# Kernel tuning notes

Hardware: AMD Instinct MI355X
Metric: run time of the kernel (lower is better)

## Reference

```python
import jax, jax.numpy as jnp
import numpy as np
from jax import lax

DN = ('NCHW', 'OIHW', 'NCHW')
BN_EPS = 1e-5
LRELU_SLOPE = 0.01


def conv_block(x, w1, b1, w2, b2, gamma, bn_bias):
    # Conv2d(512->256, k=1) -> Conv2d(256->512, k=3, pad=1) -> LeakyReLU -> BatchNorm2d(512)
    y = lax.conv_general_dilated(x, w1, (1, 1), 'VALID', dimension_numbers=DN)
    y = y + b1[None, :, None, None]
    y = lax.conv_general_dilated(y, w2, (1, 1), 'SAME', dimension_numbers=DN)
    y = y + b2[None, :, None, None]
    y = jnp.where(y > 0, y, LRELU_SLOPE * y)
    # BatchNorm2d in training mode: batch statistics over (B, H, W) per channel
    mean = jnp.mean(y, axis=(0, 2, 3))
    var = jnp.var(y, axis=(0, 2, 3))
    y = (y - mean[None, :, None, None]) * lax.rsqrt(var + BN_EPS)[None, :, None, None]
    return y * gamma[None, :, None, None] + bn_bias[None, :, None, None]


def setup_inputs() -> dict:
    key = jax.random.key(0)
    ks = jax.random.split(key, 9)
    B, C, H, W = 8, 512, 32, 32
    x = jax.random.normal(ks[0], (B, C, H, W), dtype=jnp.float32)
    x1 = jax.random.normal(ks[1], (B, C, H, W), dtype=jnp.float32)
    x2 = jax.random.normal(ks[2], (B, C, H, W), dtype=jnp.float32)
    w1 = jax.random.normal(ks[3], (256, 512, 1, 1), dtype=jnp.float32) * 0.02
    b1 = jnp.zeros((256,), dtype=jnp.float32)
    w2 = jax.random.normal(ks[4], (512, 256, 3, 3), dtype=jnp.float32) * 0.02
    b2 = jnp.zeros((512,), dtype=jnp.float32)
    gamma = jnp.ones((512,), dtype=jnp.float32)
    bn_bias = jnp.zeros((512,), dtype=jnp.float32)
    beta = jax.random.normal(ks[5], (1,), dtype=jnp.float32)  # Parameter(zeros(1)) in torch; random so output is non-trivial
    return {"x": x, "x1": x1, "x2": x2, "w1": w1, "b1": b1, "w2": w2,
            "b2": b2, "gamma": gamma, "bn_bias": bn_bias, "beta": beta}


def reference(x, x1, x2, w1, b1, w2, b2, gamma, bn_bias, beta):
    B, C, H, W = x1.shape
    N = H * W
    F1 = conv_block(x1, w1, b1, w2, b2, gamma, bn_bias).reshape(B, C, N)   # [B, C, N]
    F2 = conv_block(x2, w1, b1, w2, b2, gamma, bn_bias).reshape(B, C, N)   # [B, C, N]
    scores = jnp.einsum('bcn,bdn->bcd', F1, F2)                            # [B, C, C]
    attention = jax.nn.softmax(scores, axis=-1)
    out = jnp.einsum('bcd,bdn->bcn', attention, x.reshape(B, C, N))
    return beta * out.reshape(B, C, H, W)
```

## Files before the change

### kernel.cpp

```cpp
#include <hip/hip_runtime.h>


typedef __attribute__((ext_vector_type(8))) short bfrag;
typedef __attribute__((ext_vector_type(4))) float facc;

__device__ __forceinline__ unsigned short bf16_rn(float v) {
  unsigned u = __float_as_uint(v);
  return (unsigned short)((u + 0x7fffu + ((u >> 16) & 1u)) >> 16);
}

__device__ __forceinline__ void dma16(const void* g, const void* lds) {
  __builtin_amdgcn_global_load_lds(
      (const __attribute__((address_space(1))) unsigned int*)g,
      (__attribute__((address_space(3))) unsigned int*)(unsigned int)(unsigned long long)(const char*)lds,
      16, 0, 0);
}

__global__ __launch_bounds__(256) void prologue(
    const float* __restrict__ x1, const float* __restrict__ x2,
    const float* __restrict__ w2, unsigned char* __restrict__ x12timg,
    unsigned short* __restrict__ w2s, float* __restrict__ statsz) {
  int bid = blockIdx.x;
  int t = threadIdx.x;
  if (bid < 8192) {
    __shared__ float tile[32][33];
    int p0 = (bid & 31) * 32, ci0 = ((bid >> 5) & 15) * 32, z = bid >> 9;
    const float* src = (z < 8) ? x1 + (size_t)z * 524288 : x2 + (size_t)(z - 8) * 524288;
    {
      int ci_l = t >> 5, p_l = t & 31;
#pragma unroll
      for (int j = 0; j < 4; j++)
        tile[ci_l + 8 * j][p_l] = src[(size_t)(ci0 + ci_l + 8 * j) * 1024 + p0 + p_l];
    }
    __syncthreads();
    {
      int p_l = t >> 3, cg = (t & 7) * 4;
      unsigned short hh[4], ll[4];
#pragma unroll
      for (int j = 0; j < 4; j++) {
        float v = tile[cg + j][p_l];
        hh[j] = bf16_rn(v);
        ll[j] = bf16_rn(v - __uint_as_float((unsigned)hh[j] << 16));
      }
      int px = p0 + p_l, row = px & 127, panel = px >> 7;
      int c = ci0 + cg, kc = c >> 6, ck = (c >> 3) & 7;
      int slot = ck ^ (row & 7);
      size_t byte = (((size_t)(z * 8 + panel) * 8 + kc) * 128 + row) * 256 + slot * 16 + (c & 7) * 2;
      *(ushort4*)(x12timg + byte) = make_ushort4(hh[0], hh[1], hh[2], hh[3]);
      *(ushort4*)(x12timg + byte + 128) = make_ushort4(ll[0], ll[1], ll[2], ll[3]);
    }
  } else {
    int co = bid - 8192;
    if (co < 40) statsz[co * 256 + t] = 0.f;
    int panel = co >> 7, co_l = co & 127;
    int ch = t >> 5, ci_l = t & 31;
    int chi = ci_l >> 3, cil7 = ci_l & 7;
    const float* src = w2 + ((size_t)co * 256 + t) * 9;
#pragma unroll
    for (int tap = 0; tap < 9; tap++) {
      float v = src[tap];
      unsigned short h = bf16_rn(v);
      unsigned short l = bf16_rn(v - __uint_as_float((unsigned)h << 16));
      int dy = tap / 3, slot = tap % 3;
      int e = slot * 128 + co_l;
      size_t base = (size_t)(((panel * 8 + ch) * 3 + dy)) * 24576;
      size_t off_hi = base + e * 64 + ((chi ^ (e & 7)) << 3) + cil7;
      w2s[off_hi] = h;
      w2s[off_hi ^ 32] = l;
    }
  }
}

__global__ __launch_bounds__(256) void transpose_split_x(
    const float* __restrict__ x, unsigned char* __restrict__ img) {
  __shared__ float tile[32][33];
  int z = blockIdx.z;
  const float* src = x + (size_t)z * 524288;
  int ci0 = blockIdx.y * 32, p0 = blockIdx.x * 32;
  int t = threadIdx.x;
  {
    int ci_l = t >> 5, p_l = t & 31;
#pragma unroll
    for (int j = 0; j < 4; j++)
      tile[ci_l + 8 * j][p_l] = src[(size_t)(ci0 + ci_l + 8 * j) * 1024 + p0 + p_l];
  }
  __syncthreads();
  {
    int p_l = t >> 3, cg = (t & 7) * 4;
    unsigned short hh[4], ll[4];
#pragma unroll
    for (int j = 0; j < 4; j++) {
      float v = tile[cg + j][p_l];
      hh[j] = bf16_rn(v);
      ll[j] = bf16_rn(v - __uint_as_float((unsigned)hh[j] << 16));
    }
    int px = p0 + p_l, row = px & 127, panel = px >> 7;
    int c = ci0 + cg, kc = c >> 6, ck = (c >> 3) & 7;
    int slot = ck ^ (row & 7);
    size_t byte = (((size_t)(z * 8 + panel) * 8 + kc) * 128 + row) * 256 + slot * 16 + (c & 7) * 2;
    *(ushort4*)(img + byte) = make_ushort4(hh[0], hh[1], hh[2], hh[3]);
    *(ushort4*)(img + byte + 128) = make_ushort4(ll[0], ll[1], ll[2], ll[3]);
  }
}

template <int KTOT, int EPI, int AF32, int KSPLIT>
__global__ __launch_bounds__(256, 2) void gemm_nt(
    const void* __restrict__ Asrc, long long aZS, int aKC,
    const unsigned char* __restrict__ Bimg, long long bZS, int bKC,
    void* __restrict__ out0,
    const float* __restrict__ p0, const float* __restrict__ p1,
    const float* __restrict__ p2, const float* __restrict__ p3) {
  __shared__ __attribute__((aligned(16))) unsigned char smem[49152];
  int t = threadIdx.x;
  int z = blockIdx.z;
  int zb = z, kh = 0;
  if (KSPLIT) { zb = z & 7; kh = z >> 3; }
  int m0 = blockIdx.y * 128, n0 = blockIdx.x * 64;
  int w = t >> 6, lane = t & 63;
  int lm = lane & 15, q = lane >> 4;
  int mh = (w & 1) * 64, nh = (w >> 1) * 32;
  const unsigned char* Abase = (const unsigned char*)Asrc + (size_t)zb * aZS +
      (size_t)(m0 >> 7) * ((size_t)aKC << 15) + (size_t)w * 8192 + (size_t)lane * 16;
  const unsigned char* Bbase = Bimg + (size_t)zb * bZS +
      (size_t)(n0 >> 7) * ((size_t)bKC << 15) + (size_t)(n0 & 127) * 256 +
      (size_t)w * 4096 + (size_t)lane * 16;
  facc acc[4][2] = {};
  for (int k0 = 0; k0 < KTOT; k0 += 64) {
    int kc = (KSPLIT ? kh * (KTOT / 64) : 0) + (k0 >> 6);
    __syncthreads();
    if (AF32) {
      const float* Af = (const float*)Asrc;
#pragma unroll
      for (int j = 0; j < 8; j++) {
        int idx = t + 256 * j;
        int row = idx >> 4, c4 = idx & 15;
        float4 v = *(const float4*)(Af + (size_t)(m0 + row) * KTOT + k0 + c4 * 4);
        unsigned short h0 = bf16_rn(v.x), h1 = bf16_rn(v.y), h2 = bf16_rn(v.z), h3 = bf16_rn(v.w);
        unsigned short l0 = bf16_rn(v.x - __uint_as_float((unsigned)h0 << 16));
        unsigned short l1 = bf16_rn(v.y - __uint_as_float((unsigned)h1 << 16));
        unsigned short l2 = bf16_rn(v.z - __uint_as_float((unsigned)h2 << 16));
        unsigned short l3 = bf16_rn(v.w - __uint_as_float((unsigned)h3 << 16));
        int base = row * 256 + (((c4 >> 1) ^ (row & 7)) * 16) + (c4 & 1) * 8;
        *(ushort4*)(smem + base) = make_ushort4(h0, h1, h2, h3);
        *(ushort4*)(smem + base + 128) = make_ushort4(l0, l1, l2, l3);
      }
    } else {
      const unsigned char* ap = Abase + ((size_t)kc << 15);
#pragma unroll
      for (int j = 0; j < 8; j++) dma16(ap + j * 1024, smem + w * 8192 + j * 1024);
    }
    {
      const unsigned char* bp = Bbase + ((size_t)kc << 15);
#pragma unroll
      for (int j = 0; j < 4; j++) dma16(bp + j * 1024, smem + 32768 + w * 4096 + j * 1024);
    }
    __syncthreads();
#pragma unroll
    for (int ks = 0; ks < 2; ks++) {
      bfrag ah[4], al[4], bh[2], bl[2];
#pragma unroll
      for (int mt = 0; mt < 4; mt++) {
        int m = mh + mt * 16 + lm;
        int phys = ((ks * 4 + q) ^ (m & 7)) * 16;
        const unsigned char* p = smem + m * 256 + phys;
        ah[mt] = *(const bfrag*)p;
        al[mt] = *(const bfrag*)(p + 128);
      }
#pragma unroll
      for (int nt = 0; nt < 2; nt++) {
        int n = nh + nt * 16 + lm;
        int phys = ((ks * 4 + q) ^ (n & 7)) * 16;
        const unsigned char* p = smem + 32768 + n * 256 + phys;
        bh[nt] = *(const bfrag*)p;
        bl[nt] = *(const bfrag*)(p + 128);
      }
#pragma unroll
      for (int mt = 0; mt < 4; mt++)
#pragma unroll
        for (int nt = 0; nt < 2; nt++) {
          acc[mt][nt] = __builtin_amdgcn_mfma_f32_16x16x32_bf16(ah[mt], bh[nt], acc[mt][nt], 0, 0, 0);
          acc[mt][nt] = __builtin_amdgcn_mfma_f32_16x16x32_bf16(ah[mt], bl[nt], acc[mt][nt], 0, 0, 0);
          acc[mt][nt] = __builtin_amdgcn_mfma_f32_16x16x32_bf16(al[mt], bh[nt], acc[mt][nt], 0, 0, 0);
        }
    }
  }
  if (EPI == 0) {
    unsigned char* Yimg = (unsigned char*)out0;
    int g = zb;
#pragma unroll
    for (int mt = 0; mt < 4; mt++) {
      int mb = m0 + mh + mt * 16 + q * 4;
      int ch = mb >> 5, chunk = (mb >> 3) & 3, e2 = (mb & 7) * 2;
#pragma unroll
      for (int nt = 0; nt < 2; nt++) {
        int px = n0 + nh + nt * 16 + lm;
        int gy = px >> 5, gx = px & 31;
        int slot = chunk ^ ((gx + 1) & 7);
        size_t base = ((size_t)((g * 8 + ch) * 32 + gy)) * 4096 + gx * 128 + slot * 16 + e2;
        unsigned short hh[4], ll[4];
#pragma unroll
        for (int r = 0; r < 4; r++) {
          float v = acc[mt][nt][r] + p0[mb + r];
          hh[r] = bf16_rn(v);
          ll[r] = bf16_rn(v - __uint_as_float((unsigned)hh[r] << 16));
        }
        *(ushort4*)(Yimg + base) = make_ushort4(hh[0], hh[1], hh[2], hh[3]);
        *(ushort4*)(Yimg + (base ^ 64)) = make_ushort4(ll[0], ll[1], ll[2], ll[3]);
      }
    }
  } else if (EPI == 1) {
    float* S = (float*)out0 + (size_t)kh * 2097152;
    const float* stats = p0;
    const float* rowsum = p1;
    const float* gamma = p2;
    const float* bnb = p3;
    float a2v[2], t2v[2], r2v[2];
#pragma unroll
    for (int nt = 0; nt < 2; nt++) {
      int d = n0 + nh + nt * 16 + lm;
      float mu = stats[512 + d] * (1.f / 8192.f);
      float var = stats[1536 + d] * (1.f / 8192.f) - mu * mu;
      float a = gamma[d] * rsqrtf(var + 1e-5f);
      a2v[nt] = a;
      t2v[nt] = bnb[d] - mu * a;
      r2v[nt] = rowsum[(8 + zb) * 512 + d];
    }
#pragma unroll
    for (int mt = 0; mt < 4; mt++)
#pragma unroll
      for (int r = 0; r < 4; r++) {
        int cc = m0 + mh + mt * 16 + q * 4 + r;
        float mu = stats[cc] * (1.f / 8192.f);
        float var = stats[1024 + cc] * (1.f / 8192.f) - mu * mu;
        float a1 = gamma[cc] * rsqrtf(var + 1e-5f);
        float t1 = bnb[cc] - mu * a1;
        float r1 = rowsum[zb * 512 + cc];
#pragma unroll
        for (int nt = 0; nt < 2; nt++) {
          int d = n0 + nh + nt * 16 + lm;
          float sc = a1 * a2v[nt] * acc[mt][nt][r];
          if (kh == 0)
            sc += a1 * t2v[nt] * r1 + t1 * a2v[nt] * r2v[nt] + 1024.f * t1 * t2v[nt];
          S[((size_t)(zb * 512 + cc)) * 512 + d] = sc;
        }
      }
  } else {
    float* O = (float*)out0;
    float sc = p0[0];
#pragma unroll
    for (int mt = 0; mt < 4; mt++)
#pragma unroll
      for (int r = 0; r < 4; r++) {
        int cc = m0 + mh + mt * 16 + q * 4 + r;
#pragma unroll
        for (int nt = 0; nt < 2; nt++) {
          int n = n0 + nh + nt * 16 + lm;
          O[((size_t)(zb * 512 + cc)) * 1024 + n] = sc * acc[mt][nt][r];
        }
      }
  }
}

__global__ __launch_bounds__(256, 2) void conv3x3_mfma(
    const unsigned char* __restrict__ Yimg, const unsigned short* __restrict__ w2s,
    const float* __restrict__ b2, unsigned char* __restrict__ Fimg,
    float* __restrict__ stats, float* __restrict__ rowsum) {
  __shared__ __attribute__((aligned(16))) unsigned char smem[75264];
  const int WOFF = 26112;
  int t = threadIdx.x;
  int g = blockIdx.z;
  int panel = blockIdx.y;
  int co_base = panel * 128;
  int y0 = blockIdx.x * 4;
  int w = t >> 6, lane = t & 63;
  int lm = lane & 15, q = lane >> 4;
  int co_half = (w & 1) * 64, px_half = (w >> 1) * 64;
  int px_l[4], row_l[4], x_l[4];
#pragma unroll
  for (int i = 0; i < 4; i++) {
    px_l[i] = px_half + i * 16 + lm;
    row_l[i] = px_l[i] >> 5;
    x_l[i] = px_l[i] & 31;
  }
  for (int u = t; u < 1632; u += 256)
    *(uint4*)(smem + u * 16) = make_uint4(0u, 0u, 0u, 0u);
  const unsigned char* wgbase =
      (const unsigned char*)w2s + (size_t)panel * 8 * 3 * 49152 + w * 12288 + lane * 16;
  const unsigned char* ldsw = smem + WOFF + w * 12288;
  facc acc[4][4] = {};
  for (int chunk = 0; chunk < 8; chunk++) {
    for (int dy = 0; dy < 3; dy++) {
      __syncthreads();
      {
        const unsigned char* gsrc = wgbase + (size_t)(chunk * 3 + dy) * 49152;
#pragma unroll
        for (int j = 0; j < 12; j++) dma16(gsrc + j * 1024, ldsw + j * 1024);
      }
      if (dy == 0) {
#pragma unroll
        for (int j = 0; j < 6; j++) {
          int id = w * 6 + j;
          int strip = id >> 2, part = id & 3;
          int gy = y0 - 1 + strip;
          if ((unsigned)gy < 32u) {
            const unsigned char* src = Yimg +
                ((size_t)((g * 8 + chunk) * 32 + gy)) * 4096 + part * 1024 + lane * 16;
            dma16(src, smem + strip * 4352 + 128 + part * 1024);
          }
        }
      }
      __syncthreads();
#pragma unroll
      for (int dx = 0; dx < 3; dx++) {
        bfrag ah[4], al[4], bh[4], bl[4];
#pragma unroll
        for (int j = 0; j < 4; j++) {
          int cr = co_half + j * 16 + lm;
          const unsigned char* p = smem + WOFF + dx * 16384 + cr * 128;
          int ph = (q ^ (lm & 7)) * 16;
          ah[j] = *(const bfrag*)(p + ph);
          al[j] = *(const bfrag*)(p + (ph ^ 64));
        }
#pragma unroll
        for (int i = 0; i < 4; i++) {
          int xh = x_l[i] + dx;
          int entry = (row_l[i] + dy) * 34 + xh;
          const unsigned char* p = smem + entry * 128;
          int ph = (q ^ (xh & 7)) * 16;
          bh[i] = *(const bfrag*)(p + ph);
          bl[i] = *(const bfrag*)(p + (ph ^ 64));
        }
#pragma unroll
        for (int j = 0; j < 4; j++)
#pragma unroll
          for (int i = 0; i < 4; i++) {
            acc[j][i] = __builtin_amdgcn_mfma_f32_16x16x32_bf16(ah[j], bh[i], acc[j][i], 0, 0, 0);
            acc[j][i] = __builtin_amdgcn_mfma_f32_16x16x32_bf16(ah[j], bl[i], acc[j][i], 0, 0, 0);
            acc[j][i] = __builtin_amdgcn_mfma_f32_16x16x32_bf16(al[j], bh[i], acc[j][i], 0, 0, 0);
          }
      }
    }
  }
  int grp = g >> 3;
  int px0 = blockIdx.x * 128;
#pragma unroll
  for (int j = 0; j < 4; j++) {
#pragma unroll
    for (int r = 0; r < 4; r++) {
      int co = co_base + co_half + j * 16 + q * 4 + r;
      int row = co & 127;
      float bb = b2[co];
      float s = 0.f, s2 = 0.f;
#pragma unroll
      for (int i = 0; i < 4; i++) {
        float v = acc[j][i][r] + bb;
        v = v > 0.f ? v : 0.01f * v;
        unsigned short h = bf16_rn(v);
        unsigned short l = bf16_rn(v - __uint_as_float((unsigned)h << 16));
        int px = px0 + px_l[i];
        int kc = px >> 6, ck = (px >> 3) & 7;
        int slot = ck ^ (row & 7);
        size_t byte = (((size_t)(g * 4 + panel) * 16 + kc) * 128 + row) * 256 +
                      slot * 16 + (px & 7) * 2;
        *(unsigned short*)(Fimg + byte) = h;
        *(unsigned short*)(Fimg + byte + 128) = l;
        s += v;
        s2 = fmaf(v, v, s2);
      }
#pragma unroll
      for (int d = 1; d <= 8; d <<= 1) {
        s += __shfl_xor(s, d);
        s2 += __shfl_xor(s2, d);
      }
      if (lm == 0) {
        atomicAdd(&stats[grp * 512 + co], s);
        atomicAdd(&stats[1024 + grp * 512 + co], s2);
        atomicAdd(&rowsum[g * 512 + co], s);
      }
    }
  }
}

__global__ __launch_bounds__(256) void softmax_rows(const float* __restrict__ S,
                                                    unsigned char* __restrict__ attimg) {
  int rowg = blockIdx.x;
  int z = rowg >> 9, c = rowg & 511;
  const float* p = S + (size_t)rowg * 512;
  const float* p1 = p + 2097152;
  int t = threadIdx.x;
  float2 va = *(const float2*)(p + 2 * t);
  float2 vb = *(const float2*)(p1 + 2 * t);
  float vx = va.x + vb.x, vy = va.y + vb.y;
  float mx = fmaxf(vx, vy);
#pragma unroll
  for (int d = 32; d >= 1; d >>= 1) mx = fmaxf(mx, __shfl_xor(mx, d));
  __shared__ float sred[8];
  int wave = t >> 6, lane = t & 63;
  if (lane == 0) sred[wave] = mx;
  __syncthreads();
  float m4 = fmaxf(fmaxf(sred[0], sred[1]), fmaxf(sred[2], sred[3]));
  float ex = expf(vx - m4), ey = expf(vy - m4);
  float s = ex + ey;
#pragma unroll
  for (int d = 32; d >= 1; d >>= 1) s += __shfl_xor(s, d);
  if (lane == 0) sred[4 + wave] = s;
  __syncthreads();
  float inv = 1.f / (sred[4] + sred[5] + sred[6] + sred[7]);
  float px_ = ex * inv, py_ = ey * inv;
  unsigned short h0 = bf16_rn(px_), h1 = bf16_rn(py_);
  unsigned short l0 = bf16_rn(px_ - __uint_as_float((unsigned)h0 << 16));
  unsigned short l1 = bf16_rn(py_ - __uint_as_float((unsigned)h1 << 16));
  int rowl = c & 127, panel = c >> 7;
  int d0 = 2 * t;
  int kc = d0 >> 6, ck = (d0 >> 3) & 7;
  int slot = ck ^ (rowl & 7);
  size_t byte = (((size_t)(z * 4 + panel) * 8 + kc) * 128 + rowl) * 256 +
                slot * 16 + (d0 & 7) * 2;
  *(ushort2*)(attimg + byte) = make_ushort2(h0, h1);
  *(ushort2*)(attimg + byte + 128) = make_ushort2(l0, l1);
}

extern "C" void kernel_launch(void* const* d_in, const int* in_sizes, int n_in,
                              void* d_out, int out_size, void* d_ws, size_t ws_size,
                              hipStream_t stream) {
  const float* x = (const float*)d_in[0];
  const float* x1 = (const float*)d_in[1];
  const float* x2 = (const float*)d_in[2];
  const float* w1 = (const float*)d_in[3];
  const float* b1 = (const float*)d_in[4];
  const float* w2 = (const float*)d_in[5];
  const float* b2 = (const float*)d_in[6];
  const float* gamma = (const float*)d_in[7];
  const float* bnb = (const float*)d_in[8];
  const float* beta = (const float*)d_in[9];
  float* out = (float*)d_out;
  unsigned char* wsb = (unsigned char*)d_ws;

  unsigned char* x12timg = wsb;
  unsigned char* Fimg = wsb;
  unsigned char* xtimg = wsb;
  unsigned char* attimg = wsb + 16777216;
  unsigned char* Yimg = wsb + 33554432;
  float* S = (float*)(wsb + 33554432);
  unsigned short* w2s = (unsigned short*)(wsb + 50331648);
  float* stats = (float*)(wsb + 55050240);
  float* rowsum = (float*)(wsb + 55058432);

  prologue<<<8704, 256, 0, stream>>>(x1, x2, w2, x12timg, w2s, stats);
  gemm_nt<512, 0, 1, 0><<<dim3(16, 2, 16), 256, 0, stream>>>(
      w1, 0LL, 0, x12timg, 2097152LL, 8, Yimg, b1, nullptr, nullptr, nullptr);
  conv3x3_mfma<<<dim3(8, 4, 16), 256, 0, stream>>>(
      Yimg, w2s, b2, Fimg, stats, rowsum);
  gemm_nt<512, 1, 0, 1><<<dim3(8, 4, 16), 256, 0, stream>>>(
      Fimg, 2097152LL, 16, Fimg + (size_t)8 * 2097152, 2097152LL, 16,
      S, stats, rowsum, gamma, bnb);
  transpose_split_x<<<dim3(32, 16, 8), 256, 0, stream>>>(x, xtimg);
  softmax_rows<<<4096, 256, 0, stream>>>(S, attimg);
  gemm_nt<512, 2, 0, 0><<<dim3(16, 4, 8), 256, 0, stream>>>(
      attimg, 1048576LL, 8, xtimg, 2097152LL, 8, out, beta, nullptr, nullptr, nullptr);
}
```

Measured before the change: 287.7 us.

## Load conv3x3 weights directly from global into registers and double-buffer input tiles

The prologue now writes w2 in a fragment-native layout, so each wave can load its MFMA A-operands straight from global memory into registers instead of staging them through LDS. LDS now holds only the input halo tiles, double-buffered, with the next chunk's DMA issued mid-loop, and only one barrier per chunk instead of two per dy step. This cuts LDS traffic and barrier stalls, but makes weight loads depend on global/L2 latency and bandwidth, and the 8 register fragments add VGPR pressure.

```diff
diff --git a/kernel.cpp b/kernel.cpp
--- a/kernel.cpp
+++ b/kernel.cpp
@@ -52,21 +52,19 @@
   } else {
     int co = bid - 8192;
     if (co < 40) statsz[co * 256 + t] = 0.f;
-    int panel = co >> 7, co_l = co & 127;
-    int ch = t >> 5, ci_l = t & 31;
-    int chi = ci_l >> 3, cil7 = ci_l & 7;
+    int panel = co >> 7, coh = (co >> 6) & 1, jf = (co >> 4) & 3, lmv = co & 15;
+    int chunk = t >> 5, qv = (t >> 3) & 3, e = t & 7;
+    int lanev = qv * 16 + lmv;
     const float* src = w2 + ((size_t)co * 256 + t) * 9;
 #pragma unroll
     for (int tap = 0; tap < 9; tap++) {
       float v = src[tap];
       unsigned short h = bf16_rn(v);
       unsigned short l = bf16_rn(v - __uint_as_float((unsigned)h << 16));
-      int dy = tap / 3, slot = tap % 3;
-      int e = slot * 128 + co_l;
-      size_t base = (size_t)(((panel * 8 + ch) * 3 + dy)) * 24576;
-      size_t off_hi = base + e * 64 + ((chi ^ (e & 7)) << 3) + cil7;
-      w2s[off_hi] = h;
-      w2s[off_hi ^ 32] = l;
+      int P = (panel * 8 + chunk) * 9 + tap;
+      size_t us = (((size_t)(P * 2 + coh) * 8 + jf * 2) * 512) + lanev * 8 + e;
+      w2s[us] = h;
+      w2s[us + 512] = l;
     }
   }
 }
@@ -265,8 +263,7 @@
     const unsigned char* __restrict__ Yimg, const unsigned short* __restrict__ w2s,
     const float* __restrict__ b2, unsigned char* __restrict__ Fimg,
     float* __restrict__ stats, float* __restrict__ rowsum) {
-  __shared__ __attribute__((aligned(16))) unsigned char smem[75264];
-  const int WOFF = 26112;
+  __shared__ __attribute__((aligned(16))) unsigned char smem[2][26112];
   int t = threadIdx.x;
   int g = blockIdx.z;
   int panel = blockIdx.y;
@@ -282,64 +279,59 @@
     row_l[i] = px_l[i] >> 5;
     x_l[i] = px_l[i] & 31;
   }
-  for (int u = t; u < 1632; u += 256)
-    *(uint4*)(smem + u * 16) = make_uint4(0u, 0u, 0u, 0u);
-  const unsigned char* wgbase =
-      (const unsigned char*)w2s + (size_t)panel * 8 * 3 * 49152 + w * 12288 + lane * 16;
-  const unsigned char* ldsw = smem + WOFF + w * 12288;
+  auto stageIn = [&](int ct, unsigned char* dst) {
+#pragma unroll
+    for (int jj = 0; jj < 6; jj++) {
+      int id = w * 6 + jj;
+      int strip = id >> 2, part = id & 3;
+      int gy = y0 - 1 + strip;
+      if ((unsigned)gy < 32u) {
+        const unsigned char* srcp = Yimg +
+            ((size_t)((g * 8 + ct) * 32 + gy)) * 4096 + part * 1024 + lane * 16;
+        dma16(srcp, dst + strip * 4352 + 128 + part * 1024);
+      }
+    }
+  };
+  for (int u = t; u < 3264; u += 256)
+    *(uint4*)(&smem[0][0] + (size_t)u * 16) = make_uint4(0u, 0u, 0u, 0u);
+  __syncthreads();
+  stageIn(0, &smem[0][0]);
+  __syncthreads();
+  const unsigned char* wg0 = (const unsigned char*)w2s +
+      (size_t)panel * 72 * 16384 + (size_t)(w & 1) * 8192 + (size_t)lane * 16;
   facc acc[4][4] = {};
-  for (int chunk = 0; chunk < 8; chunk++) {
-    for (int dy = 0; dy < 3; dy++) {
-      __syncthreads();
-      {
-        const unsigned char* gsrc = wgbase + (size_t)(chunk * 3 + dy) * 49152;
-#pragma unroll
-        for (int j = 0; j < 12; j++) dma16(gsrc + j * 1024, ldsw + j * 1024);
-      }
-      if (dy == 0) {
-#pragma unroll
-        for (int j = 0; j < 6; j++) {
-          int id = w * 6 + j;
-          int strip = id >> 2, part = id & 3;
-          int gy = y0 - 1 + strip;
-          if ((unsigned)gy < 32u) {
-            const unsigned char* src = Yimg +
-                ((size_t)((g * 8 + chunk) * 32 + gy)) * 4096 + part * 1024 + lane * 16;
-            dma16(src, smem + strip * 4352 + 128 + part * 1024);
-          }
+#pragma unroll 1
+  for (int c = 0; c < 8; c++) {
+    const unsigned char* bufp = &smem[c & 1][0];
+    const unsigned char* wpc = wg0 + (((size_t)c * 9) << 14);
+#pragma unroll
+    for (int r = 0; r < 9; r++) {
+      const int dy = r / 3, dx = r % 3;
+      bfrag W[8];
+#pragma unroll
+      for (int u = 0; u < 8; u++)
+        W[u] = *(const bfrag*)(wpc + (((size_t)r) << 14) + u * 1024);
+      if (r == 3 && c < 7) stageIn(c + 1, &smem[(c + 1) & 1][0]);
+      bfrag bh[4], bl[4];
+#pragma unroll
+      for (int i = 0; i < 4; i++) {
+        int xh = x_l[i] + dx;
+        int entry = (row_l[i] + dy) * 34 + xh;
+        const unsigned char* pb = bufp + entry * 128;
+        int ph = (q ^ (xh & 7)) * 16;
+        bh[i] = *(const bfrag*)(pb + ph);
+        bl[i] = *(const bfrag*)(pb + (ph ^ 64));
+      }
+#pragma unroll
+      for (int j = 0; j < 4; j++)
+#pragma unroll
+        for (int i = 0; i < 4; i++) {
+          acc[j][i] = __builtin_amdgcn_mfma_f32_16x16x32_bf16(W[2 * j], bh[i], acc[j][i], 0, 0, 0);
+          acc[j][i] = __builtin_amdgcn_mfma_f32_16x16x32_bf16(W[2 * j], bl[i], acc[j][i], 0, 0, 0);
+          acc[j][i] = __builtin_amdgcn_mfma_f32_16x16x32_bf16(W[2 * j + 1], bh[i], acc[j][i], 0, 0, 0);
         }
-      }
-      __syncthreads();
-#pragma unroll
-      for (int dx = 0; dx < 3; dx++) {
-        bfrag ah[4], al[4], bh[4], bl[4];
-#pragma unroll
-        for (int j = 0; j < 4; j++) {
-          int cr = co_half + j * 16 + lm;
-          const unsigned char* p = smem + WOFF + dx * 16384 + cr * 128;
-          int ph = (q ^ (lm & 7)) * 16;
-          ah[j] = *(const bfrag*)(p + ph);
-          al[j] = *(const bfrag*)(p + (ph ^ 64));
-        }
-#pragma unroll
-        for (int i = 0; i < 4; i++) {
-          int xh = x_l[i] + dx;
-          int entry = (row_l[i] + dy) * 34 + xh;
-          const unsigned char* p = smem + entry * 128;
-          int ph = (q ^ (xh & 7)) * 16;
-          bh[i] = *(const bfrag*)(p + ph);
-          bl[i] = *(const bfrag*)(p + (ph ^ 64));
-        }
-#pragma unroll
-        for (int j = 0; j < 4; j++)
-#pragma unroll
-          for (int i = 0; i < 4; i++) {
-            acc[j][i] = __builtin_amdgcn_mfma_f32_16x16x32_bf16(ah[j], bh[i], acc[j][i], 0, 0, 0);
-            acc[j][i] = __builtin_amdgcn_mfma_f32_16x16x32_bf16(ah[j], bl[i], acc[j][i], 0, 0, 0);
-            acc[j][i] = __builtin_amdgcn_mfma_f32_16x16x32_bf16(al[j], bh[i], acc[j][i], 0, 0, 0);
-          }
-      }
-    }
+    }
+    __syncthreads();
   }
   int grp = g >> 3;
   int px0 = blockIdx.x * 128;
```

After: 299.0 us. +3.9%, slower.
